# Optimization experiments

Hardware: AMD Instinct MI355X
Metric: run time of the kernel (lower is better)

Reference implementation:

```python
import jax, jax.numpy as jnp
import numpy as np

B, N, C, K, COUT = 2, 16384, 64, 17, 128  # K = neighbors+self; kernel_size = K-1


def setup_inputs() -> dict:
    key = jax.random.key(0)
    kx, ka, kw = jax.random.split(key, 3)
    x = jax.random.normal(kx, (B, N, C), dtype=jnp.float32)
    # neighbor indices in [0, N), guaranteed != self via offset trick (avoids 0/0 in frame normalization)
    off = jax.random.randint(ka, (B, N, K), 1, N)
    adj = ((jnp.arange(N)[None, :, None] + off) % N).astype(jnp.int32)
    # kaiming_uniform-like init scale
    bound = 1.0 / np.sqrt(C * (K - 1))
    weight = jax.random.uniform(kw, (COUT, C, K - 1), dtype=jnp.float32, minval=-bound, maxval=bound)
    return {"x": x, "adj": adj, "weight": weight}


def reference(x, adj, weight):
    # x: [B,N,C], adj: [B,N,K] int, weight: [Cout,C,K-1]
    knn_idx = adj[:, :, 1:]                      # [B,N,K-1] drop self column
    knn = jax.vmap(lambda xb, ib: xb[ib])(x, knn_idx)   # gather -> [B,N,K-1,C]
    diff = knn - x[:, :, None, :]                # [B,N,K-1,C]
    norm = jnp.sqrt(jnp.sum(diff * diff, axis=-1, keepdims=True))   # [B,N,K-1,1]
    frame = jnp.concatenate([diff, norm], axis=-1)                  # [B,N,K-1,C+1]
    frame = frame / jnp.sqrt(jnp.sum(frame * frame, axis=-1, keepdims=True))
    radius = 1.0
    proj = radius * frame[..., :-1]              # drop norm coord -> [B,N,K-1,C]
    # per-neighbor kernel slice contraction, then ReLU and max over neighborhood
    out = jnp.einsum('ocj,bnjc->bonj', weight, proj)  # [B,Cout,N,K-1]
    out = jnp.max(jax.nn.relu(out), axis=-1)          # [B,Cout,N]
    return out
```

## Files before the change

kernel.cpp:

```cpp
#include <hip/hip_runtime.h>
#include <hip/hip_bf16.h>

typedef __attribute__((ext_vector_type(8))) short bf16x8;
typedef __attribute__((ext_vector_type(4))) float f32x4;

#define N_PTS   16384
#define C_CH    64
#define K_ADJ   17
#define C_OUT   128
#define N_J     16

__device__ __hip_bfloat16 g_wb[N_J * C_OUT * C_CH];

__global__ __launch_bounds__(256) void prep_weights_k(const float* __restrict__ w) {
    int idx = blockIdx.x * 256 + threadIdx.x;
    int c = idx & 63;
    int o = (idx >> 6) & 127;
    int j = idx >> 13;
    g_wb[idx] = __float2bfloat16(w[(o * C_CH + c) * N_J + j]);
}

__global__ __launch_bounds__(256, 2) void sconv_k(
    const float* __restrict__ x,
    const int*   __restrict__ adj,
    float*       __restrict__ out)
{
    const int p      = blockIdx.x;
    const int g8     = p & 7;
    const int b      = g8 >> 2;
    const int slot   = ((p >> 3) << 2) | (g8 & 3);

    const int lane = threadIdx.x & 63;
    const int wid  = threadIdx.x >> 6;
    const int tg   = wid & 1;
    const int oh   = wid >> 1;
    const int lrow = lane & 15;
    const int lk   = lane >> 4;
    const int cb   = lk * 8;

    const int nbase = slot * 64 + tg * 32;

    const float* __restrict__ xb   = x   + (size_t)b * N_PTS * C_CH;
    const int*   __restrict__ adjb = adj + (size_t)b * N_PTS * K_ADJ;
    float*       __restrict__ ob   = out + (size_t)b * C_OUT * N_PTS;

    int   nidx[2];
    float center[2][16];
    #pragma unroll
    for (int g = 0; g < 2; ++g) {
        const int n = nbase + g * 16 + lrow;
        nidx[g] = n;
        const float* rp = xb + n * C_CH + cb;
        const float4 v0 = *(const float4*)(rp + 0);
        const float4 v1 = *(const float4*)(rp + 4);
        const float4 v2 = *(const float4*)(rp + 32);
        const float4 v3 = *(const float4*)(rp + 36);
        center[g][0]  = v0.x; center[g][1]  = v0.y; center[g][2]  = v0.z; center[g][3]  = v0.w;
        center[g][4]  = v1.x; center[g][5]  = v1.y; center[g][6]  = v1.z; center[g][7]  = v1.w;
        center[g][8]  = v2.x; center[g][9]  = v2.y; center[g][10] = v2.z; center[g][11] = v2.w;
        center[g][12] = v3.x; center[g][13] = v3.y; center[g][14] = v3.z; center[g][15] = v3.w;
    }

    int aidx[2][N_J];
    #pragma unroll
    for (int g = 0; g < 2; ++g) {
        const int base = nidx[g] * K_ADJ + 1;
        #pragma unroll
        for (int j = 0; j < N_J; ++j) aidx[g][j] = adjb[base + j];
    }

    f32x4 maxacc[4][2];
    #pragma unroll
    for (int of = 0; of < 4; ++of)
        #pragma unroll
        for (int g = 0; g < 2; ++g)
            maxacc[of][g] = f32x4{0.f, 0.f, 0.f, 0.f};

    const __hip_bfloat16* __restrict__ wb = g_wb;

    #pragma unroll
    for (int j = 0; j < N_J; ++j) {
        bf16x8 bfrag[2][2];
        #pragma unroll
        for (int g = 0; g < 2; ++g) {
            const float* rp = xb + aidx[g][j] * C_CH + cb;
            const float4 v0 = *(const float4*)(rp + 0);
            const float4 v1 = *(const float4*)(rp + 4);
            const float4 v2 = *(const float4*)(rp + 32);
            const float4 v3 = *(const float4*)(rp + 36);
            float d[16];
            d[0]=v0.x;  d[1]=v0.y;  d[2]=v0.z;  d[3]=v0.w;
            d[4]=v1.x;  d[5]=v1.y;  d[6]=v1.z;  d[7]=v1.w;
            d[8]=v2.x;  d[9]=v2.y;  d[10]=v2.z; d[11]=v2.w;
            d[12]=v3.x; d[13]=v3.y; d[14]=v3.z; d[15]=v3.w;
            float s = 0.f;
            #pragma unroll
            for (int i = 0; i < 16; ++i) { d[i] -= center[g][i]; s = fmaf(d[i], d[i], s); }
            s += __shfl_xor(s, 16);
            s += __shfl_xor(s, 32);
            const float scale = rsqrtf(2.0f * s);
            #pragma unroll
            for (int i = 0; i < 8; ++i) {
                bfrag[g][0][i] = (short)__builtin_bit_cast(unsigned short, __float2bfloat16(d[i]     * scale));
                bfrag[g][1][i] = (short)__builtin_bit_cast(unsigned short, __float2bfloat16(d[i + 8] * scale));
            }
        }

        const __hip_bfloat16* wj = wb + j * (C_OUT * C_CH);
        #pragma unroll
        for (int of = 0; of < 4; ++of) {
            const __hip_bfloat16* wr = wj + (oh * 64 + of * 16 + lrow) * C_CH + cb;
            const bf16x8 a0 = *(const bf16x8*)(wr);
            const bf16x8 a1 = *(const bf16x8*)(wr + 32);
            #pragma unroll
            for (int g = 0; g < 2; ++g) {
                f32x4 acc = f32x4{0.f, 0.f, 0.f, 0.f};
                acc = __builtin_amdgcn_mfma_f32_16x16x32_bf16(a0, bfrag[g][0], acc, 0, 0, 0);
                acc = __builtin_amdgcn_mfma_f32_16x16x32_bf16(a1, bfrag[g][1], acc, 0, 0, 0);
                #pragma unroll
                for (int r = 0; r < 4; ++r)
                    maxacc[of][g][r] = fmaxf(maxacc[of][g][r], acc[r]);
            }
        }
    }

    #pragma unroll
    for (int of = 0; of < 4; ++of) {
        const int o0 = oh * 64 + of * 16 + lk * 4;
        #pragma unroll
        for (int g = 0; g < 2; ++g) {
            const int n = nbase + g * 16 + lrow;
            #pragma unroll
            for (int r = 0; r < 4; ++r)
                ob[(o0 + r) * N_PTS + n] = maxacc[of][g][r];
        }
    }
}

extern "C" void kernel_launch(void* const* d_in, const int* in_sizes, int n_in,
                              void* d_out, int out_size, void* d_ws, size_t ws_size,
                              hipStream_t stream) {
    (void)in_sizes; (void)n_in; (void)d_ws; (void)ws_size; (void)out_size;
    const float* x   = (const float*)d_in[0];
    const int*   adj = (const int*)d_in[1];
    const float* w   = (const float*)d_in[2];
    float*       out = (float*)d_out;

    hipLaunchKernelGGL(prep_weights_k, dim3(512), dim3(256), 0, stream, w);
    hipLaunchKernelGGL(sconv_k,        dim3(512), dim3(256), 0, stream, x, adj, out);
}
```

Measured before the change: 75.30 us.

## Halve points per wave, double grid, and software-prefetch next neighbor gather

```diff
diff --git a/kernel.cpp b/kernel.cpp
--- a/kernel.cpp
+++ b/kernel.cpp
@@ -20,15 +20,15 @@
     g_wb[idx] = __float2bfloat16(w[(o * C_CH + c) * N_J + j]);
 }
 
-__global__ __launch_bounds__(256, 2) void sconv_k(
+__global__ __launch_bounds__(256, 4) void sconv_k(
     const float* __restrict__ x,
     const int*   __restrict__ adj,
     float*       __restrict__ out)
 {
-    const int p      = blockIdx.x;
-    const int g8     = p & 7;
-    const int b      = g8 >> 2;
-    const int slot   = ((p >> 3) << 2) | (g8 & 3);
+    const int p    = blockIdx.x;
+    const int g8   = p & 7;
+    const int b    = g8 >> 2;
+    const int slot = ((p >> 3) << 2) | (g8 & 3);
 
     const int lane = threadIdx.x & 63;
     const int wid  = threadIdx.x >> 6;
@@ -38,89 +38,89 @@
     const int lk   = lane >> 4;
     const int cb   = lk * 8;
 
-    const int nbase = slot * 64 + tg * 32;
+    const int n = slot * 32 + tg * 16 + lrow;
 
     const float* __restrict__ xb   = x   + (size_t)b * N_PTS * C_CH;
     const int*   __restrict__ adjb = adj + (size_t)b * N_PTS * K_ADJ;
     float*       __restrict__ ob   = out + (size_t)b * C_OUT * N_PTS;
 
-    int   nidx[2];
-    float center[2][16];
-    #pragma unroll
-    for (int g = 0; g < 2; ++g) {
-        const int n = nbase + g * 16 + lrow;
-        nidx[g] = n;
-        const float* rp = xb + n * C_CH + cb;
+    float center[16];
+    {
+        const float* rp = xb + (size_t)n * C_CH + cb;
         const float4 v0 = *(const float4*)(rp + 0);
         const float4 v1 = *(const float4*)(rp + 4);
         const float4 v2 = *(const float4*)(rp + 32);
         const float4 v3 = *(const float4*)(rp + 36);
-        center[g][0]  = v0.x; center[g][1]  = v0.y; center[g][2]  = v0.z; center[g][3]  = v0.w;
-        center[g][4]  = v1.x; center[g][5]  = v1.y; center[g][6]  = v1.z; center[g][7]  = v1.w;
-        center[g][8]  = v2.x; center[g][9]  = v2.y; center[g][10] = v2.z; center[g][11] = v2.w;
-        center[g][12] = v3.x; center[g][13] = v3.y; center[g][14] = v3.z; center[g][15] = v3.w;
+        center[0]  = v0.x; center[1]  = v0.y; center[2]  = v0.z; center[3]  = v0.w;
+        center[4]  = v1.x; center[5]  = v1.y; center[6]  = v1.z; center[7]  = v1.w;
+        center[8]  = v2.x; center[9]  = v2.y; center[10] = v2.z; center[11] = v2.w;
+        center[12] = v3.x; center[13] = v3.y; center[14] = v3.z; center[15] = v3.w;
     }
 
-    int aidx[2][N_J];
-    #pragma unroll
-    for (int g = 0; g < 2; ++g) {
-        const int base = nidx[g] * K_ADJ + 1;
+    int aidx[N_J];
+    {
+        const int base = n * K_ADJ + 1;
         #pragma unroll
-        for (int j = 0; j < N_J; ++j) aidx[g][j] = adjb[base + j];
+        for (int j = 0; j < N_J; ++j) aidx[j] = adjb[base + j];
     }
 
-    f32x4 maxacc[4][2];
+    f32x4 maxacc[4];
     #pragma unroll
-    for (int of = 0; of < 4; ++of)
-        #pragma unroll
-        for (int g = 0; g < 2; ++g)
-            maxacc[of][g] = f32x4{0.f, 0.f, 0.f, 0.f};
+    for (int of = 0; of < 4; ++of) maxacc[of] = f32x4{0.f, 0.f, 0.f, 0.f};
 
     const __hip_bfloat16* __restrict__ wb = g_wb;
 
+    float4 p0, p1, p2, p3;
+    {
+        const float* gp = xb + (size_t)aidx[0] * C_CH + cb;
+        p0 = *(const float4*)(gp + 0);
+        p1 = *(const float4*)(gp + 4);
+        p2 = *(const float4*)(gp + 32);
+        p3 = *(const float4*)(gp + 36);
+    }
+
     #pragma unroll
     for (int j = 0; j < N_J; ++j) {
-        bf16x8 bfrag[2][2];
+        float d[16];
+        d[0]=p0.x;  d[1]=p0.y;  d[2]=p0.z;  d[3]=p0.w;
+        d[4]=p1.x;  d[5]=p1.y;  d[6]=p1.z;  d[7]=p1.w;
+        d[8]=p2.x;  d[9]=p2.y;  d[10]=p2.z; d[11]=p2.w;
+        d[12]=p3.x; d[13]=p3.y; d[14]=p3.z; d[15]=p3.w;
+
+        if (j < N_J - 1) {
+            const float* gp = xb + (size_t)aidx[j + 1] * C_CH + cb;
+            p0 = *(const float4*)(gp + 0);
+            p1 = *(const float4*)(gp + 4);
+            p2 = *(const float4*)(gp + 32);
+            p3 = *(const float4*)(gp + 36);
+        }
+
+        float s = 0.f;
         #pragma unroll
-        for (int g = 0; g < 2; ++g) {
-            const float* rp = xb + aidx[g][j] * C_CH + cb;
-            const float4 v0 = *(const float4*)(rp + 0);
-            const float4 v1 = *(const float4*)(rp + 4);
-            const float4 v2 = *(const float4*)(rp + 32);
-            const float4 v3 = *(const float4*)(rp + 36);
-            float d[16];
-            d[0]=v0.x;  d[1]=v0.y;  d[2]=v0.z;  d[3]=v0.w;
-            d[4]=v1.x;  d[5]=v1.y;  d[6]=v1.z;  d[7]=v1.w;
-            d[8]=v2.x;  d[9]=v2.y;  d[10]=v2.z; d[11]=v2.w;
-            d[12]=v3.x; d[13]=v3.y; d[14]=v3.z; d[15]=v3.w;
-            float s = 0.f;
-            #pragma unroll
-            for (int i = 0; i < 16; ++i) { d[i] -= center[g][i]; s = fmaf(d[i], d[i], s); }
-            s += __shfl_xor(s, 16);
-            s += __shfl_xor(s, 32);
-            const float scale = rsqrtf(2.0f * s);
-            #pragma unroll
-            for (int i = 0; i < 8; ++i) {
-                bfrag[g][0][i] = (short)__builtin_bit_cast(unsigned short, __float2bfloat16(d[i]     * scale));
-                bfrag[g][1][i] = (short)__builtin_bit_cast(unsigned short, __float2bfloat16(d[i + 8] * scale));
-            }
+        for (int i = 0; i < 16; ++i) { d[i] -= center[i]; s = fmaf(d[i], d[i], s); }
+        s += __shfl_xor(s, 16);
+        s += __shfl_xor(s, 32);
+        const float scale = rsqrtf(2.0f * s);
+
+        bf16x8 bf0, bf1;
+        #pragma unroll
+        for (int i = 0; i < 8; ++i) {
+            bf0[i] = (short)__builtin_bit_cast(unsigned short, __float2bfloat16(d[i]     * scale));
+            bf1[i] = (short)__builtin_bit_cast(unsigned short, __float2bfloat16(d[i + 8] * scale));
         }
 
         const __hip_bfloat16* wj = wb + j * (C_OUT * C_CH);
         #pragma unroll
         for (int of = 0; of < 4; ++of) {
-            const __hip_bfloat16* wr = wj + (oh * 64 + of * 16 + lrow) * C_CH + cb;
+            const __hip_bfloat16* wr = wj + (size_t)(oh * 64 + of * 16 + lrow) * C_CH + cb;
             const bf16x8 a0 = *(const bf16x8*)(wr);
             const bf16x8 a1 = *(const bf16x8*)(wr + 32);
+            f32x4 acc = f32x4{0.f, 0.f, 0.f, 0.f};
+            acc = __builtin_amdgcn_mfma_f32_16x16x32_bf16(a0, bf0, acc, 0, 0, 0);
+            acc = __builtin_amdgcn_mfma_f32_16x16x32_bf16(a1, bf1, acc, 0, 0, 0);
             #pragma unroll
-            for (int g = 0; g < 2; ++g) {
-                f32x4 acc = f32x4{0.f, 0.f, 0.f, 0.f};
-                acc = __builtin_amdgcn_mfma_f32_16x16x32_bf16(a0, bfrag[g][0], acc, 0, 0, 0);
-                acc = __builtin_amdgcn_mfma_f32_16x16x32_bf16(a1, bfrag[g][1], acc, 0, 0, 0);
-                #pragma unroll
-                for (int r = 0; r < 4; ++r)
-                    maxacc[of][g][r] = fmaxf(maxacc[of][g][r], acc[r]);
-            }
+            for (int r = 0; r < 4; ++r)
+                maxacc[of][r] = fmaxf(maxacc[of][r], acc[r]);
         }
     }
 
@@ -128,12 +128,8 @@
     for (int of = 0; of < 4; ++of) {
         const int o0 = oh * 64 + of * 16 + lk * 4;
         #pragma unroll
-        for (int g = 0; g < 2; ++g) {
-            const int n = nbase + g * 16 + lrow;
-            #pragma unroll
-            for (int r = 0; r < 4; ++r)
-                ob[(o0 + r) * N_PTS + n] = maxacc[of][g][r];
-        }
+        for (int r = 0; r < 4; ++r)
+            ob[(size_t)(o0 + r) * N_PTS + n] = maxacc[of][r];
     }
 }
 
@@ -146,6 +142,6 @@
     const float* w   = (const float*)d_in[2];
     float*       out = (float*)d_out;
 
-    hipLaunchKernelGGL(prep_weights_k, dim3(512), dim3(256), 0, stream, w);
-    hipLaunchKernelGGL(sconv_k,        dim3(512), dim3(256), 0, stream, x, adj, out);
+    hipLaunchKernelGGL(prep_weights_k, dim3(512),  dim3(256), 0, stream, w);
+    hipLaunchKernelGGL(sconv_k,        dim3(1024), dim3(256), 0, stream, x, adj, out);
 }
```

New measurement: 133.8 us. 77.7% more time.
